# Optimization experiments

Hardware: AMD Instinct MI355X
Metric: run time of the kernel (lower is better)

The kernel has to match this reference:

```python
import jax, jax.numpy as jnp
import numpy as np

N_NODES = 100000
N_EDGES = 1000000
NODE_DIM = 64
HIDDEN_DIM = 128


def setup_inputs() -> dict:
    key = jax.random.key(0)
    ks = jax.random.split(key, 9)
    x = jax.random.normal(ks[0], (N_NODES, NODE_DIM), dtype=jnp.float32)
    y = jax.random.normal(ks[1], (N_NODES, NODE_DIM), dtype=jnp.float32)
    edge_index = jax.random.randint(ks[2], (2, N_EDGES), 0, N_NODES, dtype=jnp.int64)
    pos_x = jax.random.normal(ks[3], (N_NODES, 3), dtype=jnp.float32)
    pos_y = jax.random.normal(ks[4], (N_NODES, 3), dtype=jnp.float32)
    in_dim = NODE_DIM * 2 + 1
    # Kaiming-uniform-ish init like torch Linear
    lim1 = 1.0 / np.sqrt(in_dim)
    lim2 = 1.0 / np.sqrt(HIDDEN_DIM)
    W1 = jax.random.uniform(ks[5], (in_dim, HIDDEN_DIM), jnp.float32, -lim1, lim1)
    b1 = jax.random.uniform(ks[6], (HIDDEN_DIM,), jnp.float32, -lim1, lim1)
    W2 = jax.random.uniform(ks[7], (HIDDEN_DIM, 1), jnp.float32, -lim2, lim2)
    b2 = jax.random.uniform(ks[8], (1,), jnp.float32, -lim2, lim2)
    return {"x": x, "y": y, "edge_index": edge_index, "pos_x": pos_x,
            "pos_y": pos_y, "W1": W1, "b1": b1, "W2": W2, "b2": b2}


def reference(x, y, edge_index, pos_x, pos_y, W1, b1, W2, b2):
    src = edge_index[0]
    dst = edge_index[1]
    # per-edge euclidean distance between endpoint positions  [E]
    d = pos_x[src] - pos_y[dst]                      # [E, 3]
    dist = jnp.sqrt(jnp.sum(d * d, axis=1))          # [E]
    # gather + concat: [E, node_dim*2 + 1]
    mlp_in = jnp.concatenate([x[src], y[dst], dist[:, None]], axis=1)
    h = jax.nn.relu(mlp_in @ W1 + b1)                # [E, hidden]
    out = jax.nn.relu(h @ W2 + b2)                   # [E, 1]
    return out
```

## Files before the change

kernel.cpp:

```cpp
#include <hip/hip_runtime.h>
#include <hip/hip_bf16.h>


constexpr int NDIM  = 64;
constexpr int HID   = 128;
constexpr int KPAD  = 136;

typedef __attribute__((ext_vector_type(8))) short  short8;
typedef __attribute__((ext_vector_type(4))) int    int4v;
typedef __attribute__((ext_vector_type(4))) float  floatx4;

__device__ __forceinline__ short f2bf(float f) {
    union { __hip_bfloat16 h; short s; } cv;
    cv.h = __float2bfloat16(f);
    return cv.s;
}

__device__ __forceinline__ int pack2(float a, float b) {
    union { __hip_bfloat162 h; int u; } cv;
    cv.h = __float22bfloat162_rn(float2{a, b});
    return cv.u;
}

__device__ __forceinline__ short8 make_afrag_f32(const float* rp) {
    const floatx4 f0 = *reinterpret_cast<const floatx4*>(rp);
    const floatx4 f1 = *reinterpret_cast<const floatx4*>(rp + 4);
    union { int4v i; short8 s8; } cv;
    cv.i.x = pack2(f0.x, f0.y);
    cv.i.y = pack2(f0.z, f0.w);
    cv.i.z = pack2(f1.x, f1.y);
    cv.i.w = pack2(f1.z, f1.w);
    return cv.s8;
}

__global__ __launch_bounds__(256) void cvt_kernel(
    const float* __restrict__ xin, const float* __restrict__ yin,
    short* __restrict__ xb, short* __restrict__ yb, int nfl)
{
    const int stride = gridDim.x * blockDim.x;
    const int n8 = nfl >> 3;
    for (int i = blockIdx.x * blockDim.x + threadIdx.x; i < n8; i += stride) {
        {
            const floatx4 f0 = *reinterpret_cast<const floatx4*>(xin + i * 8);
            const floatx4 f1 = *reinterpret_cast<const floatx4*>(xin + i * 8 + 4);
            union { int4v v; short8 s; } c;
            c.v.x = pack2(f0.x, f0.y); c.v.y = pack2(f0.z, f0.w);
            c.v.z = pack2(f1.x, f1.y); c.v.w = pack2(f1.z, f1.w);
            *reinterpret_cast<short8*>(xb + i * 8) = c.s;
        }
        {
            const floatx4 f0 = *reinterpret_cast<const floatx4*>(yin + i * 8);
            const floatx4 f1 = *reinterpret_cast<const floatx4*>(yin + i * 8 + 4);
            union { int4v v; short8 s; } c;
            c.v.x = pack2(f0.x, f0.y); c.v.y = pack2(f0.z, f0.w);
            c.v.z = pack2(f1.x, f1.y); c.v.w = pack2(f1.z, f1.w);
            *reinterpret_cast<short8*>(yb + i * 8) = c.s;
        }
    }
}

template <bool BF16GATHER>
__global__ __launch_bounds__(256, 4) void edge_mlp_kernel(
    const float* __restrict__ x, const float* __restrict__ y,
    const short* __restrict__ xb, const short* __restrict__ yb,
    const int*  __restrict__ ei, const float* __restrict__ px,
    const float* __restrict__ py, const float* __restrict__ W1,
    const float* __restrict__ b1, const float* __restrict__ W2,
    const float* __restrict__ b2, float* __restrict__ out, int E)
{
    __shared__ __align__(16) short Wt[HID * KPAD];

    const int tid = threadIdx.x;

    for (int base = 0; base < HID * HID; base += 256 * 8) {
        float f[8];
#pragma unroll
        for (int u = 0; u < 8; ++u) f[u] = W1[base + u * 256 + tid];
#pragma unroll
        for (int u = 0; u < 8; ++u) {
            int i = base + u * 256 + tid;
            Wt[(i & 127) * KPAD + (i >> 7)] = f2bf(f[u]);
        }
    }
    if (tid < HID) {
        const int n = tid;
        Wt[n * KPAD + 128] = f2bf(W1[128 * HID + n]);
        Wt[n * KPAD + 129] = f2bf(b1[n]);
#pragma unroll
        for (int j = 130; j < 136; ++j) Wt[n * KPAD + j] = 0;
    }
    __syncthreads();

    const int lane = tid & 63;
    const int wave = tid >> 6;
    const int quad = lane >> 4;
    const int lm   = lane & 15;

    float w2v[8];
#pragma unroll
    for (int t = 0; t < 8; ++t) w2v[t] = W2[t * 16 + lm];
    const float b2s = b2[0];

    const int* __restrict__ srcp = ei;
    const int* __restrict__ dstp = ei + E;

    const int sel5 = (quad == 0) ? 128 : 0;

    const int ntiles = (E + 127) / 128;
    for (int tile = blockIdx.x; tile < ntiles; tile += gridDim.x) {
        const int mb = tile * 128 + wave * 32;
        int m0 = mb + lm;       if (m0 >= E) m0 = E - 1;
        int m1 = mb + 16 + lm;  if (m1 >= E) m1 = E - 1;
        const int src0 = srcp[m0], dst0 = dstp[m0];
        const int src1 = srcp[m1], dst1 = dstp[m1];

        float dd = 0.f;
        if (lane < 32) {
            const int ps = (lane < 16) ? src0 : src1;
            const int pd = (lane < 16) ? dst0 : dst1;
            const float ax = px[ps * 3 + 0] - py[pd * 3 + 0];
            const float ay = px[ps * 3 + 1] - py[pd * 3 + 1];
            const float az = px[ps * 3 + 2] - py[pd * 3 + 2];
            dd = sqrtf(ax * ax + ay * ay + az * az);
        }
        const float dist0 = __shfl(dd, lm, 64);
        const float dist1 = __shfl(dd, lm + 16, 64);

        short8 fa[4], fb[4];
#pragma unroll
        for (int s = 0; s < 4; ++s) {
            const int kk = s * 32 + quad * 8;
            if (BF16GATHER) {
                const short* pa = (s < 2) ? (xb + src0 * NDIM + kk)
                                          : (yb + dst0 * NDIM + (kk - 64));
                const short* pb = (s < 2) ? (xb + src1 * NDIM + kk)
                                          : (yb + dst1 * NDIM + (kk - 64));
                fa[s] = *reinterpret_cast<const short8*>(pa);
                fb[s] = *reinterpret_cast<const short8*>(pb);
            } else {
                fa[s] = make_afrag_f32((s < 2) ? (x + src0 * NDIM + kk)
                                               : (y + dst0 * NDIM + (kk - 64)));
                fb[s] = make_afrag_f32((s < 2) ? (x + src1 * NDIM + kk)
                                               : (y + dst1 * NDIM + (kk - 64)));
            }
        }
        short8 fa4, fb4;
        {
            union { int4v i; short8 s8; } ca, cb;
            const int d0 = (quad == 0) ? pack2(dist0, 1.0f) : 0;
            const int d1 = (quad == 0) ? pack2(dist1, 1.0f) : 0;
            ca.i = int4v{d0, 0, 0, 0};
            cb.i = int4v{d1, 0, 0, 0};
            fa4 = ca.s8; fb4 = cb.s8;
        }

        float p0 = 0.f, p1 = 0.f, p2 = 0.f, p3 = 0.f;
        float q0 = 0.f, q1 = 0.f, q2 = 0.f, q3 = 0.f;

        int zoff = 0;
        asm volatile("" : "+v"(zoff));
        const short* wr  = Wt + zoff + lm * KPAD + quad * 8;
        const short* wr5 = Wt + zoff + lm * KPAD + sel5;

#pragma unroll
        for (int half = 0; half < 2; ++half) {
            if (half) __builtin_amdgcn_sched_barrier(0);

            floatx4 aA[4], aB[4];
#pragma unroll
            for (int u = 0; u < 4; ++u) {
                aA[u] = floatx4{0.f, 0.f, 0.f, 0.f};
                aB[u] = floatx4{0.f, 0.f, 0.f, 0.f};
            }
#pragma unroll
            for (int u = 0; u < 4; ++u) {
                const int t = half * 4 + u;
                const short* base = wr + t * (16 * KPAD);
                const short8 bg0 = *reinterpret_cast<const short8*>(base);
                const short8 bg1 = *reinterpret_cast<const short8*>(base + 32);
                const short8 bg2 = *reinterpret_cast<const short8*>(base + 64);
                const short8 bg3 = *reinterpret_cast<const short8*>(base + 96);
                const short8 bg4 = *reinterpret_cast<const short8*>(wr5 + t * (16 * KPAD));
                aA[u] = __builtin_amdgcn_mfma_f32_16x16x32_bf16(fa[0], bg0, aA[u], 0, 0, 0);
                aB[u] = __builtin_amdgcn_mfma_f32_16x16x32_bf16(fb[0], bg0, aB[u], 0, 0, 0);
                aA[u] = __builtin_amdgcn_mfma_f32_16x16x32_bf16(fa[1], bg1, aA[u], 0, 0, 0);
                aB[u] = __builtin_amdgcn_mfma_f32_16x16x32_bf16(fb[1], bg1, aB[u], 0, 0, 0);
                aA[u] = __builtin_amdgcn_mfma_f32_16x16x32_bf16(fa[2], bg2, aA[u], 0, 0, 0);
                aB[u] = __builtin_amdgcn_mfma_f32_16x16x32_bf16(fb[2], bg2, aB[u], 0, 0, 0);
                aA[u] = __builtin_amdgcn_mfma_f32_16x16x32_bf16(fa[3], bg3, aA[u], 0, 0, 0);
                aB[u] = __builtin_amdgcn_mfma_f32_16x16x32_bf16(fb[3], bg3, aB[u], 0, 0, 0);
                aA[u] = __builtin_amdgcn_mfma_f32_16x16x32_bf16(fa4,   bg4, aA[u], 0, 0, 0);
                aB[u] = __builtin_amdgcn_mfma_f32_16x16x32_bf16(fb4,   bg4, aB[u], 0, 0, 0);
            }
#pragma unroll
            for (int u = 0; u < 4; ++u) {
                const float w = w2v[half * 4 + u];
                p0 += fmaxf(aA[u][0], 0.f) * w;
                p1 += fmaxf(aA[u][1], 0.f) * w;
                p2 += fmaxf(aA[u][2], 0.f) * w;
                p3 += fmaxf(aA[u][3], 0.f) * w;
                q0 += fmaxf(aB[u][0], 0.f) * w;
                q1 += fmaxf(aB[u][1], 0.f) * w;
                q2 += fmaxf(aB[u][2], 0.f) * w;
                q3 += fmaxf(aB[u][3], 0.f) * w;
            }
        }

#pragma unroll
        for (int off = 1; off < 16; off <<= 1) {
            p0 += __shfl_xor(p0, off, 64);
            p1 += __shfl_xor(p1, off, 64);
            p2 += __shfl_xor(p2, off, 64);
            p3 += __shfl_xor(p3, off, 64);
            q0 += __shfl_xor(q0, off, 64);
            q1 += __shfl_xor(q1, off, 64);
            q2 += __shfl_xor(q2, off, 64);
            q3 += __shfl_xor(q3, off, 64);
        }
        if (lm < 4) {
            const float vA = (lm == 0) ? p0 : (lm == 1) ? p1 : (lm == 2) ? p2 : p3;
            const float vB = (lm == 0) ? q0 : (lm == 1) ? q1 : (lm == 2) ? q2 : q3;
            const int eA = mb + quad * 4 + lm;
            const int eB = mb + 16 + quad * 4 + lm;
            if (eA < E) out[eA] = fmaxf(vA + b2s, 0.f);
            if (eB < E) out[eB] = fmaxf(vB + b2s, 0.f);
        }
    }
}

extern "C" void kernel_launch(void* const* d_in, const int* in_sizes, int n_in,
                              void* d_out, int out_size, void* d_ws, size_t ws_size,
                              hipStream_t stream)
{
    const float* x  = (const float*)d_in[0];
    const float* y  = (const float*)d_in[1];
    const int*   ei = (const int*)  d_in[2];
    const float* px = (const float*)d_in[3];
    const float* py = (const float*)d_in[4];
    const float* W1 = (const float*)d_in[5];
    const float* b1 = (const float*)d_in[6];
    const float* W2 = (const float*)d_in[7];
    const float* b2 = (const float*)d_in[8];
    float* out = (float*)d_out;
    const int E = in_sizes[2] / 2;
    const int nnode_elems = in_sizes[0];

    const size_t need = (size_t)nnode_elems * 2 * sizeof(short);
    if (ws_size >= need) {
        short* xb = (short*)d_ws;
        short* yb = xb + nnode_elems;
        cvt_kernel<<<dim3(1024), dim3(256), 0, stream>>>(x, y, xb, yb, nnode_elems);
        edge_mlp_kernel<true><<<dim3(1024), dim3(256), 0, stream>>>(
            x, y, xb, yb, ei, px, py, W1, b1, W2, b2, out, E);
    } else {
        edge_mlp_kernel<false><<<dim3(1024), dim3(256), 0, stream>>>(
            x, y, nullptr, nullptr, ei, px, py, W1, b1, W2, b2, out, E);
    }
}
```

Before: 163.3 us.

## Software-pipeline edge gathers across tiles and swizzle the weight LDS layout

Restructures the persistent tile loop as a double-buffered software pipeline. The next tile's indices, positions and feature fragments are loaded while the current tile's MFMA work runs, so gather latency is hidden behind compute. It also XOR-style swizzles the bf16 W1 tile in shared memory to reduce LDS bank conflicts on the B-fragment reads. To fit the extra live registers, launch bounds drop from 4 to 3 blocks per SM and the grid shrinks from 1024 to 768 blocks, trading occupancy for explicit prefetch.

```diff
diff --git a/kernel.cpp b/kernel.cpp
--- a/kernel.cpp
+++ b/kernel.cpp
@@ -59,8 +59,158 @@
     }
 }
 
+struct IdxB  { int s0, d0, s1, d1; };
+struct PosB  { float a0, a1, a2, b0, b1, b2; };
+struct FragB { short8 fa[4]; short8 fb[4]; };
+struct Offs  { int o0, o1, o2, o3, o4; };
+
+__device__ __forceinline__ void load_idx(int tile, int wave, int lm, int E,
+    const int* __restrict__ srcp, const int* __restrict__ dstp, IdxB& I)
+{
+    const int mb = tile * 128 + wave * 32;
+    int m0 = mb + lm;       if (m0 >= E) m0 = E - 1;
+    int m1 = mb + 16 + lm;  if (m1 >= E) m1 = E - 1;
+    I.s0 = srcp[m0]; I.d0 = dstp[m0];
+    I.s1 = srcp[m1]; I.d1 = dstp[m1];
+}
+
+__device__ __forceinline__ void load_pos(const IdxB& I, int lane,
+    const float* __restrict__ px, const float* __restrict__ py, PosB& P)
+{
+    if (lane < 32) {
+        const int ps = (lane < 16) ? I.s0 : I.s1;
+        const int pd = (lane < 16) ? I.d0 : I.d1;
+        P.a0 = px[ps * 3 + 0]; P.a1 = px[ps * 3 + 1]; P.a2 = px[ps * 3 + 2];
+        P.b0 = py[pd * 3 + 0]; P.b1 = py[pd * 3 + 1]; P.b2 = py[pd * 3 + 2];
+    }
+}
+
 template <bool BF16GATHER>
-__global__ __launch_bounds__(256, 4) void edge_mlp_kernel(
+__device__ __forceinline__ void load_frags(const IdxB& I,
+    const float* __restrict__ x, const float* __restrict__ y,
+    const short* __restrict__ xb, const short* __restrict__ yb,
+    int quad, FragB& F)
+{
+#pragma unroll
+    for (int s = 0; s < 4; ++s) {
+        const int kk = s * 32 + quad * 8;
+        if (BF16GATHER) {
+            const short* pa = (s < 2) ? (xb + I.s0 * NDIM + kk)
+                                      : (yb + I.d0 * NDIM + (kk - 64));
+            const short* pb = (s < 2) ? (xb + I.s1 * NDIM + kk)
+                                      : (yb + I.d1 * NDIM + (kk - 64));
+            F.fa[s] = *reinterpret_cast<const short8*>(pa);
+            F.fb[s] = *reinterpret_cast<const short8*>(pb);
+        } else {
+            F.fa[s] = make_afrag_f32((s < 2) ? (x + I.s0 * NDIM + kk)
+                                             : (y + I.d0 * NDIM + (kk - 64)));
+            F.fb[s] = make_afrag_f32((s < 2) ? (x + I.s1 * NDIM + kk)
+                                             : (y + I.d1 * NDIM + (kk - 64)));
+        }
+    }
+}
+
+__device__ __forceinline__ void compute_tile(
+    const PosB& P, const FragB& F, int tl, int E,
+    const short* __restrict__ Wt, const Offs& O,
+    int lane, int lm, int quad, int wave,
+    const float* w2v, float b2s, float* __restrict__ out)
+{
+    float dd = 0.f;
+    if (lane < 32) {
+        const float ax = P.a0 - P.b0;
+        const float ay = P.a1 - P.b1;
+        const float az = P.a2 - P.b2;
+        dd = sqrtf(ax * ax + ay * ay + az * az);
+    }
+    const float dist0 = __shfl(dd, lm, 64);
+    const float dist1 = __shfl(dd, lm + 16, 64);
+
+    short8 fa4, fb4;
+    {
+        union { int4v i; short8 s8; } ca, cb;
+        const int d0 = (quad == 0) ? pack2(dist0, 1.0f) : 0;
+        const int d1 = (quad == 0) ? pack2(dist1, 1.0f) : 0;
+        ca.i = int4v{d0, 0, 0, 0};
+        cb.i = int4v{d1, 0, 0, 0};
+        fa4 = ca.s8; fb4 = cb.s8;
+    }
+
+    float p0 = 0.f, p1 = 0.f, p2 = 0.f, p3 = 0.f;
+    float q0 = 0.f, q1 = 0.f, q2 = 0.f, q3 = 0.f;
+
+    int zoff = 0;
+    asm volatile("" : "+v"(zoff));
+    const short* wb = Wt + zoff;
+
+#pragma unroll
+    for (int half = 0; half < 2; ++half) {
+        if (half) __builtin_amdgcn_sched_barrier(0);
+
+        floatx4 aA[4], aB[4];
+#pragma unroll
+        for (int u = 0; u < 4; ++u) {
+            aA[u] = floatx4{0.f, 0.f, 0.f, 0.f};
+            aB[u] = floatx4{0.f, 0.f, 0.f, 0.f};
+        }
+#pragma unroll
+        for (int u = 0; u < 4; ++u) {
+            const int t = half * 4 + u;
+            const short* wt = wb + t * (16 * KPAD);
+            const short8 bg0 = *reinterpret_cast<const short8*>(wt + O.o0);
+            const short8 bg1 = *reinterpret_cast<const short8*>(wt + O.o1);
+            const short8 bg2 = *reinterpret_cast<const short8*>(wt + O.o2);
+            const short8 bg3 = *reinterpret_cast<const short8*>(wt + O.o3);
+            const short8 bg4 = *reinterpret_cast<const short8*>(wt + O.o4);
+            aA[u] = __builtin_amdgcn_mfma_f32_16x16x32_bf16(F.fa[0], bg0, aA[u], 0, 0, 0);
+            aB[u] = __builtin_amdgcn_mfma_f32_16x16x32_bf16(F.fb[0], bg0, aB[u], 0, 0, 0);
+            aA[u] = __builtin_amdgcn_mfma_f32_16x16x32_bf16(F.fa[1], bg1, aA[u], 0, 0, 0);
+            aB[u] = __builtin_amdgcn_mfma_f32_16x16x32_bf16(F.fb[1], bg1, aB[u], 0, 0, 0);
+            aA[u] = __builtin_amdgcn_mfma_f32_16x16x32_bf16(F.fa[2], bg2, aA[u], 0, 0, 0);
+            aB[u] = __builtin_amdgcn_mfma_f32_16x16x32_bf16(F.fb[2], bg2, aB[u], 0, 0, 0);
+            aA[u] = __builtin_amdgcn_mfma_f32_16x16x32_bf16(F.fa[3], bg3, aA[u], 0, 0, 0);
+            aB[u] = __builtin_amdgcn_mfma_f32_16x16x32_bf16(F.fb[3], bg3, aB[u], 0, 0, 0);
+            aA[u] = __builtin_amdgcn_mfma_f32_16x16x32_bf16(fa4,     bg4, aA[u], 0, 0, 0);
+            aB[u] = __builtin_amdgcn_mfma_f32_16x16x32_bf16(fb4,     bg4, aB[u], 0, 0, 0);
+        }
+#pragma unroll
+        for (int u = 0; u < 4; ++u) {
+            const float w = w2v[half * 4 + u];
+            p0 += fmaxf(aA[u][0], 0.f) * w;
+            p1 += fmaxf(aA[u][1], 0.f) * w;
+            p2 += fmaxf(aA[u][2], 0.f) * w;
+            p3 += fmaxf(aA[u][3], 0.f) * w;
+            q0 += fmaxf(aB[u][0], 0.f) * w;
+            q1 += fmaxf(aB[u][1], 0.f) * w;
+            q2 += fmaxf(aB[u][2], 0.f) * w;
+            q3 += fmaxf(aB[u][3], 0.f) * w;
+        }
+    }
+
+#pragma unroll
+    for (int off = 1; off < 16; off <<= 1) {
+        p0 += __shfl_xor(p0, off, 64);
+        p1 += __shfl_xor(p1, off, 64);
+        p2 += __shfl_xor(p2, off, 64);
+        p3 += __shfl_xor(p3, off, 64);
+        q0 += __shfl_xor(q0, off, 64);
+        q1 += __shfl_xor(q1, off, 64);
+        q2 += __shfl_xor(q2, off, 64);
+        q3 += __shfl_xor(q3, off, 64);
+    }
+    if (lm < 4) {
+        const int mb = tl * 128 + wave * 32;
+        const float vA = (lm == 0) ? p0 : (lm == 1) ? p1 : (lm == 2) ? p2 : p3;
+        const float vB = (lm == 0) ? q0 : (lm == 1) ? q1 : (lm == 2) ? q2 : q3;
+        const int eA = mb + quad * 4 + lm;
+        const int eB = mb + 16 + quad * 4 + lm;
+        if (eA < E) out[eA] = fmaxf(vA + b2s, 0.f);
+        if (eB < E) out[eB] = fmaxf(vB + b2s, 0.f);
+    }
+}
+
+template <bool BF16GATHER>
+__global__ __launch_bounds__(256, 3) void edge_mlp_kernel(
     const float* __restrict__ x, const float* __restrict__ y,
     const short* __restrict__ xb, const short* __restrict__ yb,
     const int*  __restrict__ ei, const float* __restrict__ px,
@@ -78,8 +228,11 @@
         for (int u = 0; u < 8; ++u) f[u] = W1[base + u * 256 + tid];
 #pragma unroll
         for (int u = 0; u < 8; ++u) {
-            int i = base + u * 256 + tid;
-            Wt[(i & 127) * KPAD + (i >> 7)] = f2bf(f[u]);
+            const int i   = base + u * 256 + tid;
+            const int row = i & 127;
+            const int col = i >> 7;
+            const int p   = ((col >> 3) - 2 * (row & 7)) & 15;
+            Wt[row * KPAD + p * 8 + (col & 7)] = f2bf(f[u]);
         }
     }
     if (tid < HID) {
@@ -104,127 +257,45 @@
     const int* __restrict__ srcp = ei;
     const int* __restrict__ dstp = ei + E;
 
-    const int sel5 = (quad == 0) ? 128 : 0;
+    Offs O;
+    {
+        const int r8 = lm & 7;
+        O.o0 = lm * KPAD + (((quad +  0) - 2 * r8) & 15) * 8;
+        O.o1 = lm * KPAD + (((quad +  4) - 2 * r8) & 15) * 8;
+        O.o2 = lm * KPAD + (((quad +  8) - 2 * r8) & 15) * 8;
+        O.o3 = lm * KPAD + (((quad + 12) - 2 * r8) & 15) * 8;
+        O.o4 = lm * KPAD + 128;
+    }
 
     const int ntiles = (E + 127) / 128;
-    for (int tile = blockIdx.x; tile < ntiles; tile += gridDim.x) {
-        const int mb = tile * 128 + wave * 32;
-        int m0 = mb + lm;       if (m0 >= E) m0 = E - 1;
-        int m1 = mb + 16 + lm;  if (m1 >= E) m1 = E - 1;
-        const int src0 = srcp[m0], dst0 = dstp[m0];
-        const int src1 = srcp[m1], dst1 = dstp[m1];
-
-        float dd = 0.f;
-        if (lane < 32) {
-            const int ps = (lane < 16) ? src0 : src1;
-            const int pd = (lane < 16) ? dst0 : dst1;
-            const float ax = px[ps * 3 + 0] - py[pd * 3 + 0];
-            const float ay = px[ps * 3 + 1] - py[pd * 3 + 1];
-            const float az = px[ps * 3 + 2] - py[pd * 3 + 2];
-            dd = sqrtf(ax * ax + ay * ay + az * az);
-        }
-        const float dist0 = __shfl(dd, lm, 64);
-        const float dist1 = __shfl(dd, lm + 16, 64);
-
-        short8 fa[4], fb[4];
-#pragma unroll
-        for (int s = 0; s < 4; ++s) {
-            const int kk = s * 32 + quad * 8;
-            if (BF16GATHER) {
-                const short* pa = (s < 2) ? (xb + src0 * NDIM + kk)
-                                          : (yb + dst0 * NDIM + (kk - 64));
-                const short* pb = (s < 2) ? (xb + src1 * NDIM + kk)
-                                          : (yb + dst1 * NDIM + (kk - 64));
-                fa[s] = *reinterpret_cast<const short8*>(pa);
-                fb[s] = *reinterpret_cast<const short8*>(pb);
-            } else {
-                fa[s] = make_afrag_f32((s < 2) ? (x + src0 * NDIM + kk)
-                                               : (y + dst0 * NDIM + (kk - 64)));
-                fb[s] = make_afrag_f32((s < 2) ? (x + src1 * NDIM + kk)
-                                               : (y + dst1 * NDIM + (kk - 64)));
-            }
-        }
-        short8 fa4, fb4;
-        {
-            union { int4v i; short8 s8; } ca, cb;
-            const int d0 = (quad == 0) ? pack2(dist0, 1.0f) : 0;
-            const int d1 = (quad == 0) ? pack2(dist1, 1.0f) : 0;
-            ca.i = int4v{d0, 0, 0, 0};
-            cb.i = int4v{d1, 0, 0, 0};
-            fa4 = ca.s8; fb4 = cb.s8;
-        }
-
-        float p0 = 0.f, p1 = 0.f, p2 = 0.f, p3 = 0.f;
-        float q0 = 0.f, q1 = 0.f, q2 = 0.f, q3 = 0.f;
-
-        int zoff = 0;
-        asm volatile("" : "+v"(zoff));
-        const short* wr  = Wt + zoff + lm * KPAD + quad * 8;
-        const short* wr5 = Wt + zoff + lm * KPAD + sel5;
-
-#pragma unroll
-        for (int half = 0; half < 2; ++half) {
-            if (half) __builtin_amdgcn_sched_barrier(0);
-
-            floatx4 aA[4], aB[4];
-#pragma unroll
-            for (int u = 0; u < 4; ++u) {
-                aA[u] = floatx4{0.f, 0.f, 0.f, 0.f};
-                aB[u] = floatx4{0.f, 0.f, 0.f, 0.f};
-            }
-#pragma unroll
-            for (int u = 0; u < 4; ++u) {
-                const int t = half * 4 + u;
-                const short* base = wr + t * (16 * KPAD);
-                const short8 bg0 = *reinterpret_cast<const short8*>(base);
-                const short8 bg1 = *reinterpret_cast<const short8*>(base + 32);
-                const short8 bg2 = *reinterpret_cast<const short8*>(base + 64);
-                const short8 bg3 = *reinterpret_cast<const short8*>(base + 96);
-                const short8 bg4 = *reinterpret_cast<const short8*>(wr5 + t * (16 * KPAD));
-                aA[u] = __builtin_amdgcn_mfma_f32_16x16x32_bf16(fa[0], bg0, aA[u], 0, 0, 0);
-                aB[u] = __builtin_amdgcn_mfma_f32_16x16x32_bf16(fb[0], bg0, aB[u], 0, 0, 0);
-                aA[u] = __builtin_amdgcn_mfma_f32_16x16x32_bf16(fa[1], bg1, aA[u], 0, 0, 0);
-                aB[u] = __builtin_amdgcn_mfma_f32_16x16x32_bf16(fb[1], bg1, aB[u], 0, 0, 0);
-                aA[u] = __builtin_amdgcn_mfma_f32_16x16x32_bf16(fa[2], bg2, aA[u], 0, 0, 0);
-                aB[u] = __builtin_amdgcn_mfma_f32_16x16x32_bf16(fb[2], bg2, aB[u], 0, 0, 0);
-                aA[u] = __builtin_amdgcn_mfma_f32_16x16x32_bf16(fa[3], bg3, aA[u], 0, 0, 0);
-                aB[u] = __builtin_amdgcn_mfma_f32_16x16x32_bf16(fb[3], bg3, aB[u], 0, 0, 0);
-                aA[u] = __builtin_amdgcn_mfma_f32_16x16x32_bf16(fa4,   bg4, aA[u], 0, 0, 0);
-                aB[u] = __builtin_amdgcn_mfma_f32_16x16x32_bf16(fb4,   bg4, aB[u], 0, 0, 0);
-            }
-#pragma unroll
-            for (int u = 0; u < 4; ++u) {
-                const float w = w2v[half * 4 + u];
-                p0 += fmaxf(aA[u][0], 0.f) * w;
-                p1 += fmaxf(aA[u][1], 0.f) * w;
-                p2 += fmaxf(aA[u][2], 0.f) * w;
-                p3 += fmaxf(aA[u][3], 0.f) * w;
-                q0 += fmaxf(aB[u][0], 0.f) * w;
-                q1 += fmaxf(aB[u][1], 0.f) * w;
-                q2 += fmaxf(aB[u][2], 0.f) * w;
-                q3 += fmaxf(aB[u][3], 0.f) * w;
-            }
-        }
-
-#pragma unroll
-        for (int off = 1; off < 16; off <<= 1) {
-            p0 += __shfl_xor(p0, off, 64);
-            p1 += __shfl_xor(p1, off, 64);
-            p2 += __shfl_xor(p2, off, 64);
-            p3 += __shfl_xor(p3, off, 64);
-            q0 += __shfl_xor(q0, off, 64);
-            q1 += __shfl_xor(q1, off, 64);
-            q2 += __shfl_xor(q2, off, 64);
-            q3 += __shfl_xor(q3, off, 64);
-        }
-        if (lm < 4) {
-            const float vA = (lm == 0) ? p0 : (lm == 1) ? p1 : (lm == 2) ? p2 : p3;
-            const float vB = (lm == 0) ? q0 : (lm == 1) ? q1 : (lm == 2) ? q2 : q3;
-            const int eA = mb + quad * 4 + lm;
-            const int eB = mb + 16 + quad * 4 + lm;
-            if (eA < E) out[eA] = fmaxf(vA + b2s, 0.f);
-            if (eB < E) out[eB] = fmaxf(vB + b2s, 0.f);
-        }
+    const int step = gridDim.x;
+    int tile = blockIdx.x;
+    if (tile >= ntiles) return;
+
+    IdxB In; PosB Pc, Pn; FragB Fc, Fn;
+    {
+        IdxB I0;
+        load_idx(tile, wave, lm, E, srcp, dstp, I0);
+        load_pos(I0, lane, px, py, Pc);
+        load_frags<BF16GATHER>(I0, x, y, xb, yb, quad, Fc);
+    }
+    load_idx(tile + step, wave, lm, E, srcp, dstp, In);
+
+#pragma unroll 1
+    for (;;) {
+        load_frags<BF16GATHER>(In, x, y, xb, yb, quad, Fn);
+        load_pos(In, lane, px, py, Pn);
+        load_idx(tile + 2 * step, wave, lm, E, srcp, dstp, In);
+        compute_tile(Pc, Fc, tile, E, Wt, O, lane, lm, quad, wave, w2v, b2s, out);
+        tile += step;
+        if (tile >= ntiles) break;
+
+        load_frags<BF16GATHER>(In, x, y, xb, yb, quad, Fc);
+        load_pos(In, lane, px, py, Pc);
+        load_idx(tile + 2 * step, wave, lm, E, srcp, dstp, In);
+        compute_tile(Pn, Fn, tile, E, Wt, O, lane, lm, quad, wave, w2v, b2s, out);
+        tile += step;
+        if (tile >= ntiles) break;
     }
 }
 
@@ -250,10 +321,10 @@
         short* xb = (short*)d_ws;
         short* yb = xb + nnode_elems;
         cvt_kernel<<<dim3(1024), dim3(256), 0, stream>>>(x, y, xb, yb, nnode_elems);
-        edge_mlp_kernel<true><<<dim3(1024), dim3(256), 0, stream>>>(
+        edge_mlp_kernel<true><<<dim3(768), dim3(256), 0, stream>>>(
             x, y, xb, yb, ei, px, py, W1, b1, W2, b2, out, E);
     } else {
-        edge_mlp_kernel<false><<<dim3(1024), dim3(256), 0, stream>>>(
+        edge_mlp_kernel<false><<<dim3(768), dim3(256), 0, stream>>>(
             x, y, nullptr, nullptr, ei, px, py, W1, b1, W2, b2, out, E);
     }
 }
```

Result: slower. 182.4 us (+11.7%).

## Bucket edges by source node range and map buckets to XCDs for L2 locality

Applied to the files above, without the earlier changes.

Adds a histogram, scan and scatter pass that partitions edges into 8 buckets by source-node range, then runs a new edge MLP kernel where each block starts on the bucket matching its XCD id and claims tiles through per-bucket atomic counters. Each XCD's L2 then mostly sees one eighth of the bf16 x table, which is meant to cut gather misses. In exchange it adds four extra launches, an extra pass over the edge list that writes 12 MB of sorted indices, an indirect scattered output write, and a per-tile atomic plus barrier for dynamic scheduling.

```diff
diff --git a/kernel.cpp b/kernel.cpp
--- a/kernel.cpp
+++ b/kernel.cpp
@@ -5,6 +5,8 @@
 constexpr int NDIM  = 64;
 constexpr int HID   = 128;
 constexpr int KPAD  = 136;
+constexpr int NB    = 8;
+constexpr int M_CNT = 0, M_OFF = 8, M_CUR = 17, M_TC = 25, M_TOT = 33;
 
 typedef __attribute__((ext_vector_type(8))) short  short8;
 typedef __attribute__((ext_vector_type(4))) int    int4v;
@@ -59,6 +61,76 @@
     }
 }
 
+__global__ __launch_bounds__(64) void zero_meta_kernel(int* __restrict__ meta) {
+    if (threadIdx.x < M_TOT) meta[threadIdx.x] = 0;
+}
+
+__global__ __launch_bounds__(256) void hist_kernel(
+    const int* __restrict__ ei, int E, float inv, int* __restrict__ meta)
+{
+    __shared__ int h[NB];
+    const int tid = threadIdx.x;
+    if (tid < NB) h[tid] = 0;
+    __syncthreads();
+    const int stride = gridDim.x * blockDim.x;
+    for (int e = blockIdx.x * blockDim.x + tid; e < E; e += stride) {
+        const int s = ei[e];
+        int b = (int)((float)s * inv);
+        if (b > NB - 1) b = NB - 1;
+        atomicAdd(&h[b], 1);
+    }
+    __syncthreads();
+    if (tid < NB && h[tid] > 0) atomicAdd(&meta[M_CNT + tid], h[tid]);
+}
+
+__global__ __launch_bounds__(64) void scan_kernel(int* __restrict__ meta) {
+    if (threadIdx.x == 0) {
+        int acc = 0;
+        for (int b = 0; b < NB; ++b) {
+            meta[M_OFF + b] = acc;
+            meta[M_CUR + b] = acc;
+            acc += meta[M_CNT + b];
+        }
+        meta[M_OFF + NB] = acc;
+    }
+}
+
+__global__ __launch_bounds__(256) void scatter_kernel(
+    const int* __restrict__ ei, int E, float inv, int* __restrict__ meta,
+    int* __restrict__ sSrc, int* __restrict__ sDst, int* __restrict__ sId)
+{
+    __shared__ int h[NB], base8[NB], c2[NB];
+    const int tid = threadIdx.x;
+    const int* srcp = ei;
+    const int* dstp = ei + E;
+    int* cur = meta + M_CUR;
+    const int C  = (E + gridDim.x - 1) / gridDim.x;
+    const int lo = blockIdx.x * C;
+    const int hi = (lo + C < E) ? (lo + C) : E;
+    for (int s0 = lo; s0 < hi; s0 += 256) {
+        const int e = s0 + tid;
+        const bool valid = e < hi;
+        int s = 0, d = 0, b = 0;
+        if (tid < NB) { h[tid] = 0; c2[tid] = 0; }
+        __syncthreads();
+        if (valid) {
+            s = srcp[e]; d = dstp[e];
+            b = (int)((float)s * inv);
+            if (b > NB - 1) b = NB - 1;
+            atomicAdd(&h[b], 1);
+        }
+        __syncthreads();
+        if (tid < NB && h[tid] > 0) base8[tid] = atomicAdd(&cur[tid], h[tid]);
+        __syncthreads();
+        if (valid) {
+            const int r   = atomicAdd(&c2[b], 1);
+            const int pos = base8[b] + r;
+            sSrc[pos] = s; sDst[pos] = d; sId[pos] = e;
+        }
+        __syncthreads();
+    }
+}
+
 template <bool BF16GATHER>
 __global__ __launch_bounds__(256, 4) void edge_mlp_kernel(
     const float* __restrict__ x, const float* __restrict__ y,
@@ -69,9 +141,7 @@
     const float* __restrict__ b2, float* __restrict__ out, int E)
 {
     __shared__ __align__(16) short Wt[HID * KPAD];
-
     const int tid = threadIdx.x;
-
     for (int base = 0; base < HID * HID; base += 256 * 8) {
         float f[8];
 #pragma unroll
@@ -103,7 +173,6 @@
 
     const int* __restrict__ srcp = ei;
     const int* __restrict__ dstp = ei + E;
-
     const int sel5 = (quad == 0) ? 128 : 0;
 
     const int ntiles = (E + 127) / 128;
@@ -156,7 +225,6 @@
 
         float p0 = 0.f, p1 = 0.f, p2 = 0.f, p3 = 0.f;
         float q0 = 0.f, q1 = 0.f, q2 = 0.f, q3 = 0.f;
-
         int zoff = 0;
         asm volatile("" : "+v"(zoff));
         const short* wr  = Wt + zoff + lm * KPAD + quad * 8;
@@ -165,7 +233,6 @@
 #pragma unroll
         for (int half = 0; half < 2; ++half) {
             if (half) __builtin_amdgcn_sched_barrier(0);
-
             floatx4 aA[4], aB[4];
 #pragma unroll
             for (int u = 0; u < 4; ++u) {
@@ -228,6 +295,183 @@
     }
 }
 
+__global__ __launch_bounds__(256, 4) void edge_mlp_sorted_kernel(
+    const short* __restrict__ xb, const short* __restrict__ yb,
+    const int* __restrict__ sSrc, const int* __restrict__ sDst,
+    const int* __restrict__ sId,
+    const float* __restrict__ px, const float* __restrict__ py,
+    const float* __restrict__ W1, const float* __restrict__ b1,
+    const float* __restrict__ W2, const float* __restrict__ b2,
+    float* __restrict__ out, int E, int* meta)
+{
+    __shared__ __align__(16) short Wt[HID * KPAD];
+    __shared__ int sTile;
+    const int tid = threadIdx.x;
+
+    for (int base = 0; base < HID * HID; base += 256 * 8) {
+        float f[8];
+#pragma unroll
+        for (int u = 0; u < 8; ++u) f[u] = W1[base + u * 256 + tid];
+#pragma unroll
+        for (int u = 0; u < 8; ++u) {
+            int i = base + u * 256 + tid;
+            Wt[(i & 127) * KPAD + (i >> 7)] = f2bf(f[u]);
+        }
+    }
+    if (tid < HID) {
+        const int n = tid;
+        Wt[n * KPAD + 128] = f2bf(W1[128 * HID + n]);
+        Wt[n * KPAD + 129] = f2bf(b1[n]);
+#pragma unroll
+        for (int j = 130; j < 136; ++j) Wt[n * KPAD + j] = 0;
+    }
+    __syncthreads();
+
+    const int lane = tid & 63;
+    const int wave = tid >> 6;
+    const int quad = lane >> 4;
+    const int lm   = lane & 15;
+
+    float w2v[8];
+#pragma unroll
+    for (int t = 0; t < 8; ++t) w2v[t] = W2[t * 16 + lm];
+    const float b2s = b2[0];
+    const int sel5 = (quad == 0) ? 128 : 0;
+
+    int xcd;
+    asm volatile("s_getreg_b32 %0, hwreg(HW_REG_XCC_ID)" : "=s"(xcd));
+    xcd &= (NB - 1);
+
+    const int* off = meta + M_OFF;
+    int* tc = meta + M_TC;
+
+    for (int bb = 0; bb < NB; ++bb) {
+        const int b    = (xcd + bb) & (NB - 1);
+        const int base = off[b];
+        const int cnt  = off[b + 1] - base;
+        if (cnt <= 0) continue;
+        const int nt = (cnt + 127) >> 7;
+
+        for (;;) {
+            __syncthreads();
+            if (tid == 0) sTile = atomicAdd(&tc[b], 1);
+            __syncthreads();
+            const int t = sTile;
+            if (t >= nt) break;
+
+            const int eb   = base + t * 128 + wave * 32;
+            const int eend = base + cnt;
+            int m0 = eb + lm;       if (m0 >= eend) m0 = eend - 1;
+            int m1 = eb + 16 + lm;  if (m1 >= eend) m1 = eend - 1;
+            const int src0 = sSrc[m0], dst0 = sDst[m0];
+            const int src1 = sSrc[m1], dst1 = sDst[m1];
+
+            float dd = 0.f;
+            if (lane < 32) {
+                const int ps = (lane < 16) ? src0 : src1;
+                const int pd = (lane < 16) ? dst0 : dst1;
+                const float ax = px[ps * 3 + 0] - py[pd * 3 + 0];
+                const float ay = px[ps * 3 + 1] - py[pd * 3 + 1];
+                const float az = px[ps * 3 + 2] - py[pd * 3 + 2];
+                dd = sqrtf(ax * ax + ay * ay + az * az);
+            }
+            const float dist0 = __shfl(dd, lm, 64);
+            const float dist1 = __shfl(dd, lm + 16, 64);
+
+            short8 fa[4], fb[4];
+#pragma unroll
+            for (int s = 0; s < 4; ++s) {
+                const int kk = s * 32 + quad * 8;
+                const short* pa = (s < 2) ? (xb + src0 * NDIM + kk)
+                                          : (yb + dst0 * NDIM + (kk - 64));
+                const short* pb = (s < 2) ? (xb + src1 * NDIM + kk)
+                                          : (yb + dst1 * NDIM + (kk - 64));
+                fa[s] = *reinterpret_cast<const short8*>(pa);
+                fb[s] = *reinterpret_cast<const short8*>(pb);
+            }
+            short8 fa4, fb4;
+            {
+                union { int4v i; short8 s8; } ca, cb;
+                const int d0 = (quad == 0) ? pack2(dist0, 1.0f) : 0;
+                const int d1 = (quad == 0) ? pack2(dist1, 1.0f) : 0;
+                ca.i = int4v{d0, 0, 0, 0};
+                cb.i = int4v{d1, 0, 0, 0};
+                fa4 = ca.s8; fb4 = cb.s8;
+            }
+
+            float p0 = 0.f, p1 = 0.f, p2 = 0.f, p3 = 0.f;
+            float q0 = 0.f, q1 = 0.f, q2 = 0.f, q3 = 0.f;
+            int zoff = 0;
+            asm volatile("" : "+v"(zoff));
+            const short* wr  = Wt + zoff + lm * KPAD + quad * 8;
+            const short* wr5 = Wt + zoff + lm * KPAD + sel5;
+
+#pragma unroll
+            for (int half = 0; half < 2; ++half) {
+                if (half) __builtin_amdgcn_sched_barrier(0);
+                floatx4 aA[4], aB[4];
+#pragma unroll
+                for (int u = 0; u < 4; ++u) {
+                    aA[u] = floatx4{0.f, 0.f, 0.f, 0.f};
+                    aB[u] = floatx4{0.f, 0.f, 0.f, 0.f};
+                }
+#pragma unroll
+                for (int u = 0; u < 4; ++u) {
+                    const int t8 = half * 4 + u;
+                    const short* bp = wr + t8 * (16 * KPAD);
+                    const short8 bg0 = *reinterpret_cast<const short8*>(bp);
+                    const short8 bg1 = *reinterpret_cast<const short8*>(bp + 32);
+                    const short8 bg2 = *reinterpret_cast<const short8*>(bp + 64);
+                    const short8 bg3 = *reinterpret_cast<const short8*>(bp + 96);
+                    const short8 bg4 = *reinterpret_cast<const short8*>(wr5 + t8 * (16 * KPAD));
+                    aA[u] = __builtin_amdgcn_mfma_f32_16x16x32_bf16(fa[0], bg0, aA[u], 0, 0, 0);
+                    aB[u] = __builtin_amdgcn_mfma_f32_16x16x32_bf16(fb[0], bg0, aB[u], 0, 0, 0);
+                    aA[u] = __builtin_amdgcn_mfma_f32_16x16x32_bf16(fa[1], bg1, aA[u], 0, 0, 0);
+                    aB[u] = __builtin_amdgcn_mfma_f32_16x16x32_bf16(fb[1], bg1, aB[u], 0, 0, 0);
+                    aA[u] = __builtin_amdgcn_mfma_f32_16x16x32_bf16(fa[2], bg2, aA[u], 0, 0, 0);
+                    aB[u] = __builtin_amdgcn_mfma_f32_16x16x32_bf16(fb[2], bg2, aB[u], 0, 0, 0);
+                    aA[u] = __builtin_amdgcn_mfma_f32_16x16x32_bf16(fa[3], bg3, aA[u], 0, 0, 0);
+                    aB[u] = __builtin_amdgcn_mfma_f32_16x16x32_bf16(fb[3], bg3, aB[u], 0, 0, 0);
+                    aA[u] = __builtin_amdgcn_mfma_f32_16x16x32_bf16(fa4,   bg4, aA[u], 0, 0, 0);
+                    aB[u] = __builtin_amdgcn_mfma_f32_16x16x32_bf16(fb4,   bg4, aB[u], 0, 0, 0);
+                }
+#pragma unroll
+                for (int u = 0; u < 4; ++u) {
+                    const float w = w2v[half * 4 + u];
+                    p0 += fmaxf(aA[u][0], 0.f) * w;
+                    p1 += fmaxf(aA[u][1], 0.f) * w;
+                    p2 += fmaxf(aA[u][2], 0.f) * w;
+                    p3 += fmaxf(aA[u][3], 0.f) * w;
+                    q0 += fmaxf(aB[u][0], 0.f) * w;
+                    q1 += fmaxf(aB[u][1], 0.f) * w;
+                    q2 += fmaxf(aB[u][2], 0.f) * w;
+                    q3 += fmaxf(aB[u][3], 0.f) * w;
+                }
+            }
+
+#pragma unroll
+            for (int o = 1; o < 16; o <<= 1) {
+                p0 += __shfl_xor(p0, o, 64);
+                p1 += __shfl_xor(p1, o, 64);
+                p2 += __shfl_xor(p2, o, 64);
+                p3 += __shfl_xor(p3, o, 64);
+                q0 += __shfl_xor(q0, o, 64);
+                q1 += __shfl_xor(q1, o, 64);
+                q2 += __shfl_xor(q2, o, 64);
+                q3 += __shfl_xor(q3, o, 64);
+            }
+            if (lm < 4) {
+                const float vA = (lm == 0) ? p0 : (lm == 1) ? p1 : (lm == 2) ? p2 : p3;
+                const float vB = (lm == 0) ? q0 : (lm == 1) ? q1 : (lm == 2) ? q2 : q3;
+                const int rA = t * 128 + wave * 32 + quad * 4 + lm;
+                const int rB = rA + 16;
+                if (rA < cnt) out[sId[base + rA]] = fmaxf(vA + b2s, 0.f);
+                if (rB < cnt) out[sId[base + rB]] = fmaxf(vB + b2s, 0.f);
+            }
+        }
+    }
+}
+
 extern "C" void kernel_launch(void* const* d_in, const int* in_sizes, int n_in,
                               void* d_out, int out_size, void* d_ws, size_t ws_size,
                               hipStream_t stream)
@@ -244,9 +488,29 @@
     float* out = (float*)d_out;
     const int E = in_sizes[2] / 2;
     const int nnode_elems = in_sizes[0];
-
-    const size_t need = (size_t)nnode_elems * 2 * sizeof(short);
-    if (ws_size >= need) {
+    const int nnode = nnode_elems / NDIM;
+
+    const size_t need_xy   = (size_t)nnode_elems * 2 * sizeof(short);
+    const size_t need_sort = need_xy + (size_t)E * 3 * sizeof(int) + 4096;
+
+    if (ws_size >= need_sort) {
+        short* xb = (short*)d_ws;
+        short* yb = xb + nnode_elems;
+        int* sSrc = (int*)(yb + nnode_elems);
+        int* sDst = sSrc + E;
+        int* sId  = sDst + E;
+        int* meta = sId + E;
+        const float inv = (float)NB / (float)nnode;
+
+        cvt_kernel<<<dim3(1024), dim3(256), 0, stream>>>(x, y, xb, yb, nnode_elems);
+        zero_meta_kernel<<<dim3(1), dim3(64), 0, stream>>>(meta);
+        hist_kernel<<<dim3(512), dim3(256), 0, stream>>>(ei, E, inv, meta);
+        scan_kernel<<<dim3(1), dim3(64), 0, stream>>>(meta);
+        scatter_kernel<<<dim3(512), dim3(256), 0, stream>>>(ei, E, inv, meta,
+                                                            sSrc, sDst, sId);
+        edge_mlp_sorted_kernel<<<dim3(1024), dim3(256), 0, stream>>>(
+            xb, yb, sSrc, sDst, sId, px, py, W1, b1, W2, b2, out, E, meta);
+    } else if (ws_size >= need_xy) {
         short* xb = (short*)d_ws;
         short* yb = xb + nnode_elems;
         cvt_kernel<<<dim3(1024), dim3(256), 0, stream>>>(x, y, xb, yb, nnode_elems);
```

Result: slower. 536.5 us (+228.6%).

## Process four 16-edge sub-tiles per wave to reuse LDS weight fragments

Applied to the files above, without the earlier changes.

Each wave now handles 64 edges instead of 32 per tile iteration. Every W1 fragment loaded from LDS feeds four MFMA chains instead of two, which halves LDS weight traffic per edge and gives more independent gathers in flight. The distance computation now uses all 64 lanes instead of 32. The cost is a much larger register footprint (16 accumulators, 16 gathered fragments), so the launch bound drops to 2 blocks per CU, lowering occupancy for this latency-bound gather workload.

```diff
diff --git a/kernel.cpp b/kernel.cpp
--- a/kernel.cpp
+++ b/kernel.cpp
@@ -60,7 +60,7 @@
 }
 
 template <bool BF16GATHER>
-__global__ __launch_bounds__(256, 4) void edge_mlp_kernel(
+__global__ __launch_bounds__(256, 2) void edge_mlp_kernel(
     const float* __restrict__ x, const float* __restrict__ y,
     const short* __restrict__ xb, const short* __restrict__ yb,
     const int*  __restrict__ ei, const float* __restrict__ px,
@@ -69,7 +69,6 @@
     const float* __restrict__ b2, float* __restrict__ out, int E)
 {
     __shared__ __align__(16) short Wt[HID * KPAD];
-
     const int tid = threadIdx.x;
 
     for (int base = 0; base < HID * HID; base += 256 * 8) {
@@ -103,59 +102,62 @@
 
     const int* __restrict__ srcp = ei;
     const int* __restrict__ dstp = ei + E;
-
     const int sel5 = (quad == 0) ? 128 : 0;
 
-    const int ntiles = (E + 127) / 128;
+    const int ntiles = (E + 255) / 256;
     for (int tile = blockIdx.x; tile < ntiles; tile += gridDim.x) {
-        const int mb = tile * 128 + wave * 32;
-        int m0 = mb + lm;       if (m0 >= E) m0 = E - 1;
-        int m1 = mb + 16 + lm;  if (m1 >= E) m1 = E - 1;
-        const int src0 = srcp[m0], dst0 = dstp[m0];
-        const int src1 = srcp[m1], dst1 = dstp[m1];
-
-        float dd = 0.f;
-        if (lane < 32) {
-            const int ps = (lane < 16) ? src0 : src1;
-            const int pd = (lane < 16) ? dst0 : dst1;
-            const float ax = px[ps * 3 + 0] - py[pd * 3 + 0];
-            const float ay = px[ps * 3 + 1] - py[pd * 3 + 1];
-            const float az = px[ps * 3 + 2] - py[pd * 3 + 2];
+        const int mb = tile * 256 + wave * 64;
+
+        int S[4], D[4];
+#pragma unroll
+        for (int s = 0; s < 4; ++s) {
+            int m = mb + s * 16 + lm;
+            if (m >= E) m = E - 1;
+            S[s] = srcp[m]; D[s] = dstp[m];
+        }
+
+        const int sq = (quad == 0) ? S[0] : (quad == 1) ? S[1] : (quad == 2) ? S[2] : S[3];
+        const int dq = (quad == 0) ? D[0] : (quad == 1) ? D[1] : (quad == 2) ? D[2] : D[3];
+        float dd;
+        {
+            const float ax = px[sq * 3 + 0] - py[dq * 3 + 0];
+            const float ay = px[sq * 3 + 1] - py[dq * 3 + 1];
+            const float az = px[sq * 3 + 2] - py[dq * 3 + 2];
             dd = sqrtf(ax * ax + ay * ay + az * az);
         }
-        const float dist0 = __shfl(dd, lm, 64);
-        const float dist1 = __shfl(dd, lm + 16, 64);
-
-        short8 fa[4], fb[4];
+        float di[4];
+#pragma unroll
+        for (int s = 0; s < 4; ++s) di[s] = __shfl(dd, s * 16 + lm, 64);
+
+        short8 fr[4][4];
 #pragma unroll
         for (int s = 0; s < 4; ++s) {
-            const int kk = s * 32 + quad * 8;
-            if (BF16GATHER) {
-                const short* pa = (s < 2) ? (xb + src0 * NDIM + kk)
-                                          : (yb + dst0 * NDIM + (kk - 64));
-                const short* pb = (s < 2) ? (xb + src1 * NDIM + kk)
-                                          : (yb + dst1 * NDIM + (kk - 64));
-                fa[s] = *reinterpret_cast<const short8*>(pa);
-                fb[s] = *reinterpret_cast<const short8*>(pb);
-            } else {
-                fa[s] = make_afrag_f32((s < 2) ? (x + src0 * NDIM + kk)
-                                               : (y + dst0 * NDIM + (kk - 64)));
-                fb[s] = make_afrag_f32((s < 2) ? (x + src1 * NDIM + kk)
-                                               : (y + dst1 * NDIM + (kk - 64)));
-            }
-        }
-        short8 fa4, fb4;
-        {
-            union { int4v i; short8 s8; } ca, cb;
-            const int d0 = (quad == 0) ? pack2(dist0, 1.0f) : 0;
-            const int d1 = (quad == 0) ? pack2(dist1, 1.0f) : 0;
-            ca.i = int4v{d0, 0, 0, 0};
-            cb.i = int4v{d1, 0, 0, 0};
-            fa4 = ca.s8; fb4 = cb.s8;
-        }
-
-        float p0 = 0.f, p1 = 0.f, p2 = 0.f, p3 = 0.f;
-        float q0 = 0.f, q1 = 0.f, q2 = 0.f, q3 = 0.f;
+#pragma unroll
+            for (int c = 0; c < 4; ++c) {
+                const int kk = c * 32 + quad * 8;
+                if (BF16GATHER) {
+                    const short* p = (c < 2) ? (xb + S[s] * NDIM + kk)
+                                             : (yb + D[s] * NDIM + (kk - 64));
+                    fr[s][c] = *reinterpret_cast<const short8*>(p);
+                } else {
+                    fr[s][c] = make_afrag_f32((c < 2) ? (x + S[s] * NDIM + kk)
+                                                      : (y + D[s] * NDIM + (kk - 64)));
+                }
+            }
+        }
+        short8 f4[4];
+#pragma unroll
+        for (int s = 0; s < 4; ++s) {
+            union { int4v i; short8 s8; } cc;
+            cc.i = int4v{(quad == 0) ? pack2(di[s], 1.0f) : 0, 0, 0, 0};
+            f4[s] = cc.s8;
+        }
+
+        float pv[4][4];
+#pragma unroll
+        for (int s = 0; s < 4; ++s)
+#pragma unroll
+            for (int r = 0; r < 4; ++r) pv[s][r] = 0.f;
 
         int zoff = 0;
         asm volatile("" : "+v"(zoff));
@@ -165,65 +167,62 @@
 #pragma unroll
         for (int half = 0; half < 2; ++half) {
             if (half) __builtin_amdgcn_sched_barrier(0);
-
-            floatx4 aA[4], aB[4];
-#pragma unroll
-            for (int u = 0; u < 4; ++u) {
-                aA[u] = floatx4{0.f, 0.f, 0.f, 0.f};
-                aB[u] = floatx4{0.f, 0.f, 0.f, 0.f};
-            }
+            floatx4 ac[4][4];
+#pragma unroll
+            for (int s = 0; s < 4; ++s)
+#pragma unroll
+                for (int u = 0; u < 4; ++u) ac[s][u] = floatx4{0.f, 0.f, 0.f, 0.f};
+
 #pragma unroll
             for (int u = 0; u < 4; ++u) {
                 const int t = half * 4 + u;
-                const short* base = wr + t * (16 * KPAD);
-                const short8 bg0 = *reinterpret_cast<const short8*>(base);
-                const short8 bg1 = *reinterpret_cast<const short8*>(base + 32);
-                const short8 bg2 = *reinterpret_cast<const short8*>(base + 64);
-                const short8 bg3 = *reinterpret_cast<const short8*>(base + 96);
+                const short* bp = wr + t * (16 * KPAD);
+                const short8 bg0 = *reinterpret_cast<const short8*>(bp);
+                const short8 bg1 = *reinterpret_cast<const short8*>(bp + 32);
+                const short8 bg2 = *reinterpret_cast<const short8*>(bp + 64);
+                const short8 bg3 = *reinterpret_cast<const short8*>(bp + 96);
                 const short8 bg4 = *reinterpret_cast<const short8*>(wr5 + t * (16 * KPAD));
-                aA[u] = __builtin_amdgcn_mfma_f32_16x16x32_bf16(fa[0], bg0, aA[u], 0, 0, 0);
-                aB[u] = __builtin_amdgcn_mfma_f32_16x16x32_bf16(fb[0], bg0, aB[u], 0, 0, 0);
-                aA[u] = __builtin_amdgcn_mfma_f32_16x16x32_bf16(fa[1], bg1, aA[u], 0, 0, 0);
-                aB[u] = __builtin_amdgcn_mfma_f32_16x16x32_bf16(fb[1], bg1, aB[u], 0, 0, 0);
-                aA[u] = __builtin_amdgcn_mfma_f32_16x16x32_bf16(fa[2], bg2, aA[u], 0, 0, 0);
-                aB[u] = __builtin_amdgcn_mfma_f32_16x16x32_bf16(fb[2], bg2, aB[u], 0, 0, 0);
-                aA[u] = __builtin_amdgcn_mfma_f32_16x16x32_bf16(fa[3], bg3, aA[u], 0, 0, 0);
-                aB[u] = __builtin_amdgcn_mfma_f32_16x16x32_bf16(fb[3], bg3, aB[u], 0, 0, 0);
-                aA[u] = __builtin_amdgcn_mfma_f32_16x16x32_bf16(fa4,   bg4, aA[u], 0, 0, 0);
-                aB[u] = __builtin_amdgcn_mfma_f32_16x16x32_bf16(fb4,   bg4, aB[u], 0, 0, 0);
+#pragma unroll
+                for (int s = 0; s < 4; ++s) {
+                    ac[s][u] = __builtin_amdgcn_mfma_f32_16x16x32_bf16(fr[s][0], bg0, ac[s][u], 0, 0, 0);
+                    ac[s][u] = __builtin_amdgcn_mfma_f32_16x16x32_bf16(fr[s][1], bg1, ac[s][u], 0, 0, 0);
+                    ac[s][u] = __builtin_amdgcn_mfma_f32_16x16x32_bf16(fr[s][2], bg2, ac[s][u], 0, 0, 0);
+                    ac[s][u] = __builtin_amdgcn_mfma_f32_16x16x32_bf16(fr[s][3], bg3, ac[s][u], 0, 0, 0);
+                    ac[s][u] = __builtin_amdgcn_mfma_f32_16x16x32_bf16(f4[s],    bg4, ac[s][u], 0, 0, 0);
+                }
             }
 #pragma unroll
             for (int u = 0; u < 4; ++u) {
                 const float w = w2v[half * 4 + u];
-                p0 += fmaxf(aA[u][0], 0.f) * w;
-                p1 += fmaxf(aA[u][1], 0.f) * w;
-                p2 += fmaxf(aA[u][2], 0.f) * w;
-                p3 += fmaxf(aA[u][3], 0.f) * w;
-                q0 += fmaxf(aB[u][0], 0.f) * w;
-                q1 += fmaxf(aB[u][1], 0.f) * w;
-                q2 += fmaxf(aB[u][2], 0.f) * w;
-                q3 += fmaxf(aB[u][3], 0.f) * w;
+#pragma unroll
+                for (int s = 0; s < 4; ++s) {
+                    pv[s][0] += fmaxf(ac[s][u][0], 0.f) * w;
+                    pv[s][1] += fmaxf(ac[s][u][1], 0.f) * w;
+                    pv[s][2] += fmaxf(ac[s][u][2], 0.f) * w;
+                    pv[s][3] += fmaxf(ac[s][u][3], 0.f) * w;
+                }
             }
         }
 
 #pragma unroll
         for (int off = 1; off < 16; off <<= 1) {
-            p0 += __shfl_xor(p0, off, 64);
-            p1 += __shfl_xor(p1, off, 64);
-            p2 += __shfl_xor(p2, off, 64);
-            p3 += __shfl_xor(p3, off, 64);
-            q0 += __shfl_xor(q0, off, 64);
-            q1 += __shfl_xor(q1, off, 64);
-            q2 += __shfl_xor(q2, off, 64);
-            q3 += __shfl_xor(q3, off, 64);
-        }
+#pragma unroll
+            for (int s = 0; s < 4; ++s) {
+                pv[s][0] += __shfl_xor(pv[s][0], off, 64);
+                pv[s][1] += __shfl_xor(pv[s][1], off, 64);
+                pv[s][2] += __shfl_xor(pv[s][2], off, 64);
+                pv[s][3] += __shfl_xor(pv[s][3], off, 64);
+            }
+        }
+
         if (lm < 4) {
-            const float vA = (lm == 0) ? p0 : (lm == 1) ? p1 : (lm == 2) ? p2 : p3;
-            const float vB = (lm == 0) ? q0 : (lm == 1) ? q1 : (lm == 2) ? q2 : q3;
-            const int eA = mb + quad * 4 + lm;
-            const int eB = mb + 16 + quad * 4 + lm;
-            if (eA < E) out[eA] = fmaxf(vA + b2s, 0.f);
-            if (eB < E) out[eB] = fmaxf(vB + b2s, 0.f);
+#pragma unroll
+            for (int s = 0; s < 4; ++s) {
+                const float v = (lm == 0) ? pv[s][0] : (lm == 1) ? pv[s][1]
+                              : (lm == 2) ? pv[s][2] : pv[s][3];
+                const int e = mb + s * 16 + quad * 4 + lm;
+                if (e < E) out[e] = fmaxf(v + b2s, 0.f);
+            }
         }
     }
 }
```

After: 199.4 us. 22.1% more time.
